# Optimization experiments

Measured on AMD Instinct MI355X. Metric: run time of the kernel, lower is better.

## Reference

```python
import jax, jax.numpy as jnp
import numpy as np

H = 128  # hidden size
IN = 12  # input size
OUT = 4  # output classes


def _lstm_scan(gates_x, Whh, B, dtype, collect_ys):
    """gates_x: [T,B,4H] precomputed input-to-hidden gates (with biases).
    PyTorch gate order: i, f, g, o."""
    h0 = jnp.zeros((B, H), dtype)
    c0 = jnp.zeros((B, H), dtype)

    def step(carry, gx):
        h, c = carry
        g = gx + h @ Whh.T  # [B,4H]
        i, f, gg, o = jnp.split(g, 4, axis=-1)
        c = jax.nn.sigmoid(f) * c + jax.nn.sigmoid(i) * jnp.tanh(gg)
        h = jax.nn.sigmoid(o) * jnp.tanh(c)
        return (h, c), (h if collect_ys else None)

    (hT, cT), hs = jax.lax.scan(step, (h0, c0), gates_x)
    return hs, hT


def setup_inputs() -> dict:
    key = jax.random.key(0)
    ks = jax.random.split(key, 12)
    B, T = 256, 2048
    s = 1.0 / np.sqrt(H)  # torch LSTM/Linear init scale
    u = lambda k, shape: jax.random.uniform(k, shape, jnp.float32, -s, s)
    return {
        "x": jax.random.normal(ks[0], (B, T, IN), jnp.float32),
        "W_ih_l0": u(ks[1], (4 * H, IN)),
        "W_hh_l0": u(ks[2], (4 * H, H)),
        "b_ih_l0": u(ks[3], (4 * H,)),
        "b_hh_l0": u(ks[4], (4 * H,)),
        "W_ih_l1": u(ks[5], (4 * H, H)),
        "W_hh_l1": u(ks[6], (4 * H, H)),
        "b_ih_l1": u(ks[7], (4 * H,)),
        "b_hh_l1": u(ks[8], (4 * H,)),
        "W_out": u(ks[9], (OUT, H)),
        "b_out": u(ks[10], (OUT,)),
    }


def reference(x, W_ih_l0, W_hh_l0, b_ih_l0, b_hh_l0,
              W_ih_l1, W_hh_l1, b_ih_l1, b_hh_l1, W_out, b_out):
    B = x.shape[0]
    # layer 0: precompute all input projections at once -> [T,B,4H]
    gx0 = jnp.einsum('bti,gi->tbg', x, W_ih_l0) + b_ih_l0 + b_hh_l0
    hs0, _ = _lstm_scan(gx0, W_hh_l0, B, x.dtype, collect_ys=True)  # [T,B,H]
    # layer 1: only final hidden state is needed (r_out[:, -1] == h_T)
    gx1 = jnp.einsum('tbh,gh->tbg', hs0, W_ih_l1) + b_ih_l1 + b_hh_l1
    _, hT = _lstm_scan(gx1, W_hh_l1, B, x.dtype, collect_ys=False)  # [B,H]
    return hT @ W_out.T + b_out  # [B,4]
```

## Files before the change

kernel.cpp:

```cpp
#include <hip/hip_runtime.h>
#include <cstdint>
#include <cstddef>

#define H      128
#define IN_    12
#define GATES  512
#define B_     256
#define T_     2048
#define TCMAX  512
#define TS     32


__device__ __forceinline__ float sigmoidf_(float x) {
    return 1.f / (1.f + __expf(-x));
}
__device__ __forceinline__ float tanhf_(float x) {
    return 2.f / (1.f + __expf(-2.f * x)) - 1.f;
}

__global__ __launch_bounds__(512, 1) void lstm_l0(
    const float* __restrict__ x, const float* __restrict__ Wih,
    const float* __restrict__ Whh, const float* __restrict__ bih,
    const float* __restrict__ bhh, float* __restrict__ hs0,
    float* __restrict__ state, int tc, int chunk)
{
    const int b = blockIdx.x;
    const int g = threadIdx.x;

    __shared__ alignas(16) float sh_x[TCMAX * IN_];
    __shared__ alignas(16) float sh_h[H];
    __shared__ alignas(16) float sh_act[GATES];

    float wh[H];
    const float4* wr = (const float4*)(Whh + (size_t)g * H);
#pragma unroll
    for (int k = 0; k < H / 4; ++k) {
        float4 v = wr[k];
        wh[4*k] = v.x; wh[4*k+1] = v.y; wh[4*k+2] = v.z; wh[4*k+3] = v.w;
    }
    float wi[IN_];
    const float4* wr2 = (const float4*)(Wih + (size_t)g * IN_);
#pragma unroll
    for (int k = 0; k < IN_ / 4; ++k) {
        float4 v = wr2[k];
        wi[4*k] = v.x; wi[4*k+1] = v.y; wi[4*k+2] = v.z; wi[4*k+3] = v.w;
    }
    const float bias = bih[g] + bhh[g];

    const float* xs = x + ((size_t)b * T_ + (size_t)chunk * tc) * IN_;
    for (int i = g; i < tc * IN_; i += 512) sh_x[i] = xs[i];

    float hreg = 0.f, creg = 0.f;
    if (g < H) {
        if (chunk) { hreg = state[b * 2 * H + g]; creg = state[b * 2 * H + H + g]; }
        sh_h[g] = hreg;
    }
    __syncthreads();

    float* hs_out = hs0 + (size_t)b * tc * H;

    for (int t = 0; t < tc; ++t) {
        float a0 = bias, a1 = 0.f, a2 = 0.f, a3 = 0.f;
        const float4* xh = (const float4*)(sh_x + t * IN_);
        {
            float4 v = xh[0];
            a0 = fmaf(wi[0], v.x, a0); a1 = fmaf(wi[1], v.y, a1);
            a2 = fmaf(wi[2], v.z, a2); a3 = fmaf(wi[3], v.w, a3);
            v = xh[1];
            a0 = fmaf(wi[4], v.x, a0); a1 = fmaf(wi[5], v.y, a1);
            a2 = fmaf(wi[6], v.z, a2); a3 = fmaf(wi[7], v.w, a3);
            v = xh[2];
            a0 = fmaf(wi[8], v.x, a0); a1 = fmaf(wi[9], v.y, a1);
            a2 = fmaf(wi[10], v.z, a2); a3 = fmaf(wi[11], v.w, a3);
        }
        const float4* h4 = (const float4*)sh_h;
#pragma unroll
        for (int k = 0; k < H / 4; ++k) {
            float4 v = h4[k];
            a0 = fmaf(wh[4*k],   v.x, a0); a1 = fmaf(wh[4*k+1], v.y, a1);
            a2 = fmaf(wh[4*k+2], v.z, a2); a3 = fmaf(wh[4*k+3], v.w, a3);
        }
        float pre = (a0 + a1) + (a2 + a3);
        float act = ((g >> 7) == 2) ? tanhf_(pre) : sigmoidf_(pre);
        sh_act[g] = act;
        __syncthreads();
        if (g < H) {
            creg = fmaf(sh_act[H + g], creg, sh_act[g] * sh_act[2 * H + g]);
            hreg = sh_act[3 * H + g] * tanhf_(creg);
            sh_h[g] = hreg;
            hs_out[(size_t)t * H + g] = hreg;
        }
        __syncthreads();
    }
    if (g < H) { state[b * 2 * H + g] = hreg; state[b * 2 * H + H + g] = creg; }
}

__global__ __launch_bounds__(512, 1) void lstm_l1(
    const float* __restrict__ hs0, const float* __restrict__ Wih,
    const float* __restrict__ Whh, const float* __restrict__ bih,
    const float* __restrict__ bhh, float* __restrict__ state,
    int tc, int chunk)
{
    const int b = blockIdx.x;
    const int g = threadIdx.x;

    __shared__ alignas(16) float sh_h0[TS * H];
    __shared__ alignas(16) float sh_gx[TS * GATES];
    __shared__ alignas(16) float sh_h[H];
    __shared__ alignas(16) float sh_act[GATES];

    float wh[H];
    const float4* wr = (const float4*)(Whh + (size_t)g * H);
#pragma unroll
    for (int k = 0; k < H / 4; ++k) {
        float4 v = wr[k];
        wh[4*k] = v.x; wh[4*k+1] = v.y; wh[4*k+2] = v.z; wh[4*k+3] = v.w;
    }
    const float bias = bih[g] + bhh[g];

    float hreg = 0.f, creg = 0.f;
    if (g < H) {
        if (chunk) { hreg = state[b * 2 * H + g]; creg = state[b * 2 * H + H + g]; }
        sh_h[g] = hreg;
    }
    __syncthreads();

    const float* hsrc = hs0 + (size_t)b * tc * H;
    const float4* wihrow = (const float4*)(Wih + (size_t)g * H);

    const int nsub = tc / TS;
    for (int s = 0; s < nsub; ++s) {
        const float4* src4 = (const float4*)(hsrc + (size_t)s * TS * H);
        float4* dst4 = (float4*)sh_h0;
        for (int i = g; i < TS * H / 4; i += 512) dst4[i] = src4[i];
        __syncthreads();

        float acc[TS];
#pragma unroll
        for (int t = 0; t < TS; ++t) acc[t] = bias;
        for (int k = 0; k < H / 4; ++k) {
            float4 w = wihrow[k];
            const float* hb = sh_h0 + 4 * k;
#pragma unroll
            for (int t = 0; t < TS; ++t) {
                float4 hv = *(const float4*)(hb + t * H);
                acc[t] = fmaf(w.x, hv.x,
                         fmaf(w.y, hv.y,
                         fmaf(w.z, hv.z,
                         fmaf(w.w, hv.w, acc[t]))));
            }
        }
#pragma unroll
        for (int t = 0; t < TS; ++t) sh_gx[t * GATES + g] = acc[t];
        __syncthreads();

        for (int t = 0; t < TS; ++t) {
            float a0 = sh_gx[t * GATES + g], a1 = 0.f, a2 = 0.f, a3 = 0.f;
            const float4* h4 = (const float4*)sh_h;
#pragma unroll
            for (int k = 0; k < H / 4; ++k) {
                float4 v = h4[k];
                a0 = fmaf(wh[4*k],   v.x, a0); a1 = fmaf(wh[4*k+1], v.y, a1);
                a2 = fmaf(wh[4*k+2], v.z, a2); a3 = fmaf(wh[4*k+3], v.w, a3);
            }
            float pre = (a0 + a1) + (a2 + a3);
            float act = ((g >> 7) == 2) ? tanhf_(pre) : sigmoidf_(pre);
            sh_act[g] = act;
            __syncthreads();
            if (g < H) {
                creg = fmaf(sh_act[H + g], creg, sh_act[g] * sh_act[2 * H + g]);
                hreg = sh_act[3 * H + g] * tanhf_(creg);
                sh_h[g] = hreg;
            }
            __syncthreads();
        }
    }
    if (g < H) { state[b * 2 * H + g] = hreg; state[b * 2 * H + H + g] = creg; }
}

__global__ void out_proj(const float* __restrict__ state1,
                         const float* __restrict__ Wout,
                         const float* __restrict__ bout,
                         float* __restrict__ out)
{
    const int b = blockIdx.x, j = threadIdx.x;
    __shared__ float sh[H];
    if (j < H) sh[j] = state1[b * 2 * H + j];
    __syncthreads();
    if (j < 4) {
        float a = bout[j];
        for (int k = 0; k < H; ++k) a = fmaf(Wout[j * H + k], sh[k], a);
        out[b * 4 + j] = a;
    }
}

extern "C" void kernel_launch(void* const* d_in, const int* in_sizes, int n_in,
                              void* d_out, int out_size, void* d_ws, size_t ws_size,
                              hipStream_t stream)
{
    const float* x    = (const float*)d_in[0];
    const float* Wih0 = (const float*)d_in[1];
    const float* Whh0 = (const float*)d_in[2];
    const float* bih0 = (const float*)d_in[3];
    const float* bhh0 = (const float*)d_in[4];
    const float* Wih1 = (const float*)d_in[5];
    const float* Whh1 = (const float*)d_in[6];
    const float* bih1 = (const float*)d_in[7];
    const float* bhh1 = (const float*)d_in[8];
    const float* Wout = (const float*)d_in[9];
    const float* bout = (const float*)d_in[10];

    int tc = 32;
    for (int cand = TCMAX; cand >= 32; cand >>= 1) {
        size_t need = (size_t)B_ * cand * H * 4 + (size_t)B_ * 2 * H * 4 * 2;
        if (need <= ws_size) { tc = cand; break; }
    }

    float* ws  = (float*)d_ws;
    float* hs0 = ws;
    float* st0 = ws + (size_t)B_ * tc * H;
    float* st1 = st0 + (size_t)B_ * 2 * H;

    const int nchunks = T_ / tc;
    for (int c = 0; c < nchunks; ++c) {
        lstm_l0<<<B_, 512, 0, stream>>>(x, Wih0, Whh0, bih0, bhh0, hs0, st0, tc, c);
        lstm_l1<<<B_, 512, 0, stream>>>(hs0, Wih1, Whh1, bih1, bhh1, st1, tc, c);
    }
    out_proj<<<B_, 128, 0, stream>>>(st1, Wout, bout, (float*)d_out);
}
```

Baseline: 5.747 ms.

## Broadcast hidden state via readlane instead of LDS reads in LSTM kernels

In the recurrent step, each wave now reads the hidden state once as a float2 per lane and broadcasts elements with `__builtin_amdgcn_readlane`. This replaces 32 LDS float4 broadcast reads per step, which sit on the serial critical path. The layer-1 input projection drops its `sh_h0` shared staging and the barrier that followed it. Instead, each lane loads one hidden element per timestep and the values are broadcast with readlane into 32 named accumulators. It trades LDS latency for many more scalar readlane instructions and higher register pressure, with waves_per_eu pinned to 2.

```diff
diff --git a/kernel.cpp b/kernel.cpp
--- a/kernel.cpp
+++ b/kernel.cpp
@@ -10,6 +10,17 @@
 #define TCMAX  512
 #define TS     32
 
+#define REP32(M) M(0) M(1) M(2) M(3) M(4) M(5) M(6) M(7) M(8) M(9) M(10) M(11) \
+  M(12) M(13) M(14) M(15) M(16) M(17) M(18) M(19) M(20) M(21) M(22) M(23) \
+  M(24) M(25) M(26) M(27) M(28) M(29) M(30) M(31)
+
+#define RLF(v, l) __int_as_float(__builtin_amdgcn_readlane(__float_as_int(v), (l)))
+
+#define QUAD(j) { \
+    float s0 = RLF(hl.x, 2*j), s1 = RLF(hl.y, 2*j); \
+    float s2 = RLF(hl.x, 2*j+1), s3 = RLF(hl.y, 2*j+1); \
+    a0 = fmaf(w##j.x, s0, a0); a1 = fmaf(w##j.y, s1, a1); \
+    a2 = fmaf(w##j.z, s2, a2); a3 = fmaf(w##j.w, s3, a3); }
 
 __device__ __forceinline__ float sigmoidf_(float x) {
     return 1.f / (1.f + __expf(-x));
@@ -18,33 +29,26 @@
     return 2.f / (1.f + __expf(-2.f * x)) - 1.f;
 }
 
-__global__ __launch_bounds__(512, 1) void lstm_l0(
-    const float* __restrict__ x, const float* __restrict__ Wih,
-    const float* __restrict__ Whh, const float* __restrict__ bih,
-    const float* __restrict__ bhh, float* __restrict__ hs0,
-    float* __restrict__ state, int tc, int chunk)
+__global__ __launch_bounds__(512)
+__attribute__((amdgpu_waves_per_eu(2, 2)))
+void lstm_l0(const float* __restrict__ x, const float* __restrict__ Wih,
+             const float* __restrict__ Whh, const float* __restrict__ bih,
+             const float* __restrict__ bhh, float* __restrict__ hs0,
+             float* __restrict__ state, int tc, int chunk)
 {
     const int b = blockIdx.x;
     const int g = threadIdx.x;
+    const int lane = g & 63;
 
     __shared__ alignas(16) float sh_x[TCMAX * IN_];
-    __shared__ alignas(16) float sh_h[H];
-    __shared__ alignas(16) float sh_act[GATES];
-
-    float wh[H];
-    const float4* wr = (const float4*)(Whh + (size_t)g * H);
-#pragma unroll
-    for (int k = 0; k < H / 4; ++k) {
-        float4 v = wr[k];
-        wh[4*k] = v.x; wh[4*k+1] = v.y; wh[4*k+2] = v.z; wh[4*k+3] = v.w;
-    }
-    float wi[IN_];
+    __shared__ alignas(8)  float sh_h[H];
+    __shared__ float sh_act[GATES];
+
+#define LW(j) float4 w##j = ((const float4*)(Whh + (size_t)g * H))[j];
+    REP32(LW)
+#undef LW
     const float4* wr2 = (const float4*)(Wih + (size_t)g * IN_);
-#pragma unroll
-    for (int k = 0; k < IN_ / 4; ++k) {
-        float4 v = wr2[k];
-        wi[4*k] = v.x; wi[4*k+1] = v.y; wi[4*k+2] = v.z; wi[4*k+3] = v.w;
-    }
+    float4 wiA = wr2[0], wiB = wr2[1], wiC = wr2[2];
     const float bias = bih[g] + bhh[g];
 
     const float* xs = x + ((size_t)b * T_ + (size_t)chunk * tc) * IN_;
@@ -60,26 +64,17 @@
     float* hs_out = hs0 + (size_t)b * tc * H;
 
     for (int t = 0; t < tc; ++t) {
+        float2 hl = ((const float2*)sh_h)[lane];
         float a0 = bias, a1 = 0.f, a2 = 0.f, a3 = 0.f;
         const float4* xh = (const float4*)(sh_x + t * IN_);
-        {
-            float4 v = xh[0];
-            a0 = fmaf(wi[0], v.x, a0); a1 = fmaf(wi[1], v.y, a1);
-            a2 = fmaf(wi[2], v.z, a2); a3 = fmaf(wi[3], v.w, a3);
-            v = xh[1];
-            a0 = fmaf(wi[4], v.x, a0); a1 = fmaf(wi[5], v.y, a1);
-            a2 = fmaf(wi[6], v.z, a2); a3 = fmaf(wi[7], v.w, a3);
-            v = xh[2];
-            a0 = fmaf(wi[8], v.x, a0); a1 = fmaf(wi[9], v.y, a1);
-            a2 = fmaf(wi[10], v.z, a2); a3 = fmaf(wi[11], v.w, a3);
-        }
-        const float4* h4 = (const float4*)sh_h;
-#pragma unroll
-        for (int k = 0; k < H / 4; ++k) {
-            float4 v = h4[k];
-            a0 = fmaf(wh[4*k],   v.x, a0); a1 = fmaf(wh[4*k+1], v.y, a1);
-            a2 = fmaf(wh[4*k+2], v.z, a2); a3 = fmaf(wh[4*k+3], v.w, a3);
-        }
+        float4 xv0 = xh[0], xv1 = xh[1], xv2 = xh[2];
+        a0 = fmaf(wiA.x, xv0.x, a0); a1 = fmaf(wiA.y, xv0.y, a1);
+        a2 = fmaf(wiA.z, xv0.z, a2); a3 = fmaf(wiA.w, xv0.w, a3);
+        a0 = fmaf(wiB.x, xv1.x, a0); a1 = fmaf(wiB.y, xv1.y, a1);
+        a2 = fmaf(wiB.z, xv1.z, a2); a3 = fmaf(wiB.w, xv1.w, a3);
+        a0 = fmaf(wiC.x, xv2.x, a0); a1 = fmaf(wiC.y, xv2.y, a1);
+        a2 = fmaf(wiC.z, xv2.z, a2); a3 = fmaf(wiC.w, xv2.w, a3);
+        REP32(QUAD)
         float pre = (a0 + a1) + (a2 + a3);
         float act = ((g >> 7) == 2) ? tanhf_(pre) : sigmoidf_(pre);
         sh_act[g] = act;
@@ -95,27 +90,24 @@
     if (g < H) { state[b * 2 * H + g] = hreg; state[b * 2 * H + H + g] = creg; }
 }
 
-__global__ __launch_bounds__(512, 1) void lstm_l1(
-    const float* __restrict__ hs0, const float* __restrict__ Wih,
-    const float* __restrict__ Whh, const float* __restrict__ bih,
-    const float* __restrict__ bhh, float* __restrict__ state,
-    int tc, int chunk)
+__global__ __launch_bounds__(512)
+__attribute__((amdgpu_waves_per_eu(2, 2)))
+void lstm_l1(const float* __restrict__ hs0, const float* __restrict__ Wih,
+             const float* __restrict__ Whh, const float* __restrict__ bih,
+             const float* __restrict__ bhh, float* __restrict__ state,
+             int tc, int chunk)
 {
     const int b = blockIdx.x;
     const int g = threadIdx.x;
-
-    __shared__ alignas(16) float sh_h0[TS * H];
-    __shared__ alignas(16) float sh_gx[TS * GATES];
-    __shared__ alignas(16) float sh_h[H];
-    __shared__ alignas(16) float sh_act[GATES];
-
-    float wh[H];
-    const float4* wr = (const float4*)(Whh + (size_t)g * H);
-#pragma unroll
-    for (int k = 0; k < H / 4; ++k) {
-        float4 v = wr[k];
-        wh[4*k] = v.x; wh[4*k+1] = v.y; wh[4*k+2] = v.z; wh[4*k+3] = v.w;
-    }
+    const int lane = g & 63;
+
+    __shared__ float sh_gx[TS * GATES];
+    __shared__ alignas(8) float sh_h[H];
+    __shared__ float sh_act[GATES];
+
+#define LW(j) float4 w##j = ((const float4*)(Whh + (size_t)g * H))[j];
+    REP32(LW)
+#undef LW
     const float bias = bih[g] + bhh[g];
 
     float hreg = 0.f, creg = 0.f;
@@ -128,41 +120,49 @@
     const float* hsrc = hs0 + (size_t)b * tc * H;
     const float4* wihrow = (const float4*)(Wih + (size_t)g * H);
 
-    const int nsub = tc / TS;
-    for (int s = 0; s < nsub; ++s) {
-        const float4* src4 = (const float4*)(hsrc + (size_t)s * TS * H);
-        float4* dst4 = (float4*)sh_h0;
-        for (int i = g; i < TS * H / 4; i += 512) dst4[i] = src4[i];
-        __syncthreads();
-
-        float acc[TS];
-#pragma unroll
-        for (int t = 0; t < TS; ++t) acc[t] = bias;
-        for (int k = 0; k < H / 4; ++k) {
-            float4 w = wihrow[k];
-            const float* hb = sh_h0 + 4 * k;
-#pragma unroll
-            for (int t = 0; t < TS; ++t) {
-                float4 hv = *(const float4*)(hb + t * H);
-                acc[t] = fmaf(w.x, hv.x,
-                         fmaf(w.y, hv.y,
-                         fmaf(w.z, hv.z,
-                         fmaf(w.w, hv.w, acc[t]))));
-            }
-        }
-#pragma unroll
-        for (int t = 0; t < TS; ++t) sh_gx[t * GATES + g] = acc[t];
-        __syncthreads();
+    for (int s = 0; s < tc / TS; ++s) {
+        const float* hsA = hsrc + (size_t)s * TS * H;
+
+#define DECL(t) float dA##t;
+        REP32(DECL)
+#undef DECL
+#define ACC(t) float ac##t = bias;
+        REP32(ACC)
+#undef ACC
+#define LTA(t) dA##t = hsA[t * H + lane];
+        REP32(LTA)
+#undef LTA
+        for (int k4 = 0; k4 < 16; ++k4) {
+            float4 wq = wihrow[k4];
+            int kl = 4 * k4;
+#define PA(t) { ac##t = fmaf(wq.x, RLF(dA##t, kl),     ac##t); \
+                ac##t = fmaf(wq.y, RLF(dA##t, kl + 1), ac##t); \
+                ac##t = fmaf(wq.z, RLF(dA##t, kl + 2), ac##t); \
+                ac##t = fmaf(wq.w, RLF(dA##t, kl + 3), ac##t); }
+            REP32(PA)
+#undef PA
+        }
+#define LTB(t) dA##t = hsA[t * H + 64 + lane];
+        REP32(LTB)
+#undef LTB
+        for (int k4 = 16; k4 < 32; ++k4) {
+            float4 wq = wihrow[k4];
+            int kl = 4 * k4 - 64;
+#define PB(t) { ac##t = fmaf(wq.x, RLF(dA##t, kl),     ac##t); \
+                ac##t = fmaf(wq.y, RLF(dA##t, kl + 1), ac##t); \
+                ac##t = fmaf(wq.z, RLF(dA##t, kl + 2), ac##t); \
+                ac##t = fmaf(wq.w, RLF(dA##t, kl + 3), ac##t); }
+            REP32(PB)
+#undef PB
+        }
+#define ST(t) sh_gx[t * GATES + g] = ac##t;
+        REP32(ST)
+#undef ST
 
         for (int t = 0; t < TS; ++t) {
+            float2 hl = ((const float2*)sh_h)[lane];
             float a0 = sh_gx[t * GATES + g], a1 = 0.f, a2 = 0.f, a3 = 0.f;
-            const float4* h4 = (const float4*)sh_h;
-#pragma unroll
-            for (int k = 0; k < H / 4; ++k) {
-                float4 v = h4[k];
-                a0 = fmaf(wh[4*k],   v.x, a0); a1 = fmaf(wh[4*k+1], v.y, a1);
-                a2 = fmaf(wh[4*k+2], v.z, a2); a3 = fmaf(wh[4*k+3], v.w, a3);
-            }
+            REP32(QUAD)
             float pre = (a0 + a1) + (a2 + a3);
             float act = ((g >> 7) == 2) ? tanhf_(pre) : sigmoidf_(pre);
             sh_act[g] = act;
```

Result: slower. 7.427 ms (+29.2%).

## Split recurrent matvec over 1024 threads and move layer-1 input GEMM to separate kernel

Applied to the files above, without the earlier changes.

The recurrent scan kernel now uses 1024 threads per batch row. Each thread computes a 16-wide K-slice partial for four gate rows, and the partials are reduced through padded shared memory by 128 threads, which also apply the fused gate activations. The layer-1 input projection moves out of the serial scan into a separate gx1_gemm kernel gridded over batch and time tiles, writing a gx workspace that the scan prefetches one step ahead. This cuts per-thread serial FMA depth on the recurrence critical path. In exchange it adds a shared-memory reduction each step, extra global traffic for gx1, and a larger workspace that may shrink the chunk size.

```diff
diff --git a/kernel.cpp b/kernel.cpp
--- a/kernel.cpp
+++ b/kernel.cpp
@@ -8,8 +8,12 @@
 #define B_     256
 #define T_     2048
 #define TCMAX  512
-#define TS     32
-
+#define TI     32
+#define PS     520
+
+#define REP32(M) M(0) M(1) M(2) M(3) M(4) M(5) M(6) M(7) M(8) M(9) M(10) M(11) \
+  M(12) M(13) M(14) M(15) M(16) M(17) M(18) M(19) M(20) M(21) M(22) M(23) \
+  M(24) M(25) M(26) M(27) M(28) M(29) M(30) M(31)
 
 __device__ __forceinline__ float sigmoidf_(float x) {
     return 1.f / (1.f + __expf(-x));
@@ -17,165 +21,167 @@
 __device__ __forceinline__ float tanhf_(float x) {
     return 2.f / (1.f + __expf(-2.f * x)) - 1.f;
 }
-
-__global__ __launch_bounds__(512, 1) void lstm_l0(
-    const float* __restrict__ x, const float* __restrict__ Wih,
-    const float* __restrict__ Whh, const float* __restrict__ bih,
-    const float* __restrict__ bhh, float* __restrict__ hs0,
-    float* __restrict__ state, int tc, int chunk)
-{
-    const int b = blockIdx.x;
-    const int g = threadIdx.x;
-
-    __shared__ alignas(16) float sh_x[TCMAX * IN_];
-    __shared__ alignas(16) float sh_h[H];
-    __shared__ alignas(16) float sh_act[GATES];
-
-    float wh[H];
-    const float4* wr = (const float4*)(Whh + (size_t)g * H);
-#pragma unroll
-    for (int k = 0; k < H / 4; ++k) {
-        float4 v = wr[k];
-        wh[4*k] = v.x; wh[4*k+1] = v.y; wh[4*k+2] = v.z; wh[4*k+3] = v.w;
-    }
-    float wi[IN_];
-    const float4* wr2 = (const float4*)(Wih + (size_t)g * IN_);
-#pragma unroll
-    for (int k = 0; k < IN_ / 4; ++k) {
-        float4 v = wr2[k];
-        wi[4*k] = v.x; wi[4*k+1] = v.y; wi[4*k+2] = v.z; wi[4*k+3] = v.w;
-    }
-    const float bias = bih[g] + bhh[g];
-
-    const float* xs = x + ((size_t)b * T_ + (size_t)chunk * tc) * IN_;
-    for (int i = g; i < tc * IN_; i += 512) sh_x[i] = xs[i];
-
+__device__ __forceinline__ float dot4f(float4 w, float4 h, float a) {
+    return fmaf(w.x, h.x, fmaf(w.y, h.y, fmaf(w.z, h.z, fmaf(w.w, h.w, a))));
+}
+
+template<bool IS_L0>
+__global__ __launch_bounds__(1024) void lstm_scan(
+    const float* __restrict__ x_or_gx,
+    const float* __restrict__ Wih,
+    const float* __restrict__ Whh,
+    const float* __restrict__ bih, const float* __restrict__ bhh,
+    float* __restrict__ hs0,
+    float* __restrict__ state,
+    int tc, int chunk)
+{
+    const int b   = blockIdx.x;
+    const int tid = threadIdx.x;
+    const int ks  = tid >> 7;
+    const int q   = tid & 127;
+
+    extern __shared__ float smem[];
+    float* sh_part = smem;
+    float* sh_h    = smem + 8 * PS;
+    float* sh_x    = sh_h + H;
+
+#define LOADW(i) \
+    const float4* wr##i = (const float4*)(Whh + (size_t)(4*q+i)*H + 16*ks); \
+    float4 w##i##0 = wr##i[0], w##i##1 = wr##i[1], w##i##2 = wr##i[2], w##i##3 = wr##i[3];
+    LOADW(0) LOADW(1) LOADW(2) LOADW(3)
+#undef LOADW
+
+    float4 wx0 = {0,0,0,0}, wx1 = {0,0,0,0}, wx2 = {0,0,0,0}, wx3 = {0,0,0,0};
+    if constexpr (IS_L0) {
+        if (ks >= 1 && ks <= 3) {
+            wx0 = *(const float4*)(Wih + (size_t)(4*q+0)*IN_ + 4*(ks-1));
+            wx1 = *(const float4*)(Wih + (size_t)(4*q+1)*IN_ + 4*(ks-1));
+            wx2 = *(const float4*)(Wih + (size_t)(4*q+2)*IN_ + 4*(ks-1));
+            wx3 = *(const float4*)(Wih + (size_t)(4*q+3)*IN_ + 4*(ks-1));
+        }
+        const float* xs = x_or_gx + ((size_t)b * T_ + (size_t)chunk * tc) * IN_;
+        for (int i = tid; i < tc * IN_; i += 1024) sh_x[i] = xs[i];
+    }
+
+    float bias0 = 0, bias1 = 0, bias2 = 0, bias3 = 0;
+    float cur0 = 0, cur1 = 0, cur2 = 0, cur3 = 0;
     float hreg = 0.f, creg = 0.f;
-    if (g < H) {
-        if (chunk) { hreg = state[b * 2 * H + g]; creg = state[b * 2 * H + H + g]; }
-        sh_h[g] = hreg;
+    const float* gxb = nullptr;
+    if constexpr (!IS_L0) gxb = x_or_gx + (size_t)b * tc * GATES;
+
+    if (tid < H) {
+        if constexpr (IS_L0) {
+            bias0 = bih[tid]         + bhh[tid];
+            bias1 = bih[tid + 128]   + bhh[tid + 128];
+            bias2 = bih[tid + 256]   + bhh[tid + 256];
+            bias3 = bih[tid + 384]   + bhh[tid + 384];
+        } else {
+            cur0 = gxb[tid]; cur1 = gxb[tid + 128];
+            cur2 = gxb[tid + 256]; cur3 = gxb[tid + 384];
+        }
+        if (chunk) { hreg = state[b*2*H + tid]; creg = state[b*2*H + H + tid]; }
+        sh_h[tid] = hreg;
     }
     __syncthreads();
 
-    float* hs_out = hs0 + (size_t)b * tc * H;
+    float* hs_out = nullptr;
+    if constexpr (IS_L0) hs_out = hs0 + (size_t)b * tc * H;
+
+    const float4* sh4 = (const float4*)sh_h;
+    const int i0 = tid & 3, q0 = tid >> 2;
 
     for (int t = 0; t < tc; ++t) {
-        float a0 = bias, a1 = 0.f, a2 = 0.f, a3 = 0.f;
-        const float4* xh = (const float4*)(sh_x + t * IN_);
-        {
-            float4 v = xh[0];
-            a0 = fmaf(wi[0], v.x, a0); a1 = fmaf(wi[1], v.y, a1);
-            a2 = fmaf(wi[2], v.z, a2); a3 = fmaf(wi[3], v.w, a3);
-            v = xh[1];
-            a0 = fmaf(wi[4], v.x, a0); a1 = fmaf(wi[5], v.y, a1);
-            a2 = fmaf(wi[6], v.z, a2); a3 = fmaf(wi[7], v.w, a3);
-            v = xh[2];
-            a0 = fmaf(wi[8], v.x, a0); a1 = fmaf(wi[9], v.y, a1);
-            a2 = fmaf(wi[10], v.z, a2); a3 = fmaf(wi[11], v.w, a3);
-        }
-        const float4* h4 = (const float4*)sh_h;
-#pragma unroll
-        for (int k = 0; k < H / 4; ++k) {
-            float4 v = h4[k];
-            a0 = fmaf(wh[4*k],   v.x, a0); a1 = fmaf(wh[4*k+1], v.y, a1);
-            a2 = fmaf(wh[4*k+2], v.z, a2); a3 = fmaf(wh[4*k+3], v.w, a3);
-        }
-        float pre = (a0 + a1) + (a2 + a3);
-        float act = ((g >> 7) == 2) ? tanhf_(pre) : sigmoidf_(pre);
-        sh_act[g] = act;
+        float n0 = 0, n1 = 0, n2 = 0, n3 = 0;
+        if constexpr (!IS_L0) {
+            if (tid < H) {
+                int tn = (t + 1 < tc) ? t + 1 : t;
+                const float* gp = gxb + (size_t)tn * GATES;
+                n0 = gp[tid]; n1 = gp[tid + 128];
+                n2 = gp[tid + 256]; n3 = gp[tid + 384];
+            }
+        }
+        float4 hA = sh4[4*ks], hB = sh4[4*ks+1], hC = sh4[4*ks+2], hD = sh4[4*ks+3];
+        float a0 = dot4f(w03,hD, dot4f(w02,hC, dot4f(w01,hB, dot4f(w00,hA, 0.f))));
+        float a1 = dot4f(w13,hD, dot4f(w12,hC, dot4f(w11,hB, dot4f(w10,hA, 0.f))));
+        float a2 = dot4f(w23,hD, dot4f(w22,hC, dot4f(w21,hB, dot4f(w20,hA, 0.f))));
+        float a3 = dot4f(w33,hD, dot4f(w32,hC, dot4f(w31,hB, dot4f(w30,hA, 0.f))));
+        if constexpr (IS_L0) {
+            if (ks >= 1 && ks <= 3) {
+                float4 xq = *(const float4*)(sh_x + t * IN_ + 4*(ks-1));
+                a0 = dot4f(wx0, xq, a0); a1 = dot4f(wx1, xq, a1);
+                a2 = dot4f(wx2, xq, a2); a3 = dot4f(wx3, xq, a3);
+            }
+        }
+        sh_part[ks*PS + 0*128 + q] = a0;
+        sh_part[ks*PS + 1*128 + q] = a1;
+        sh_part[ks*PS + 2*128 + q] = a2;
+        sh_part[ks*PS + 3*128 + q] = a3;
         __syncthreads();
-        if (g < H) {
-            creg = fmaf(sh_act[H + g], creg, sh_act[g] * sh_act[2 * H + g]);
-            hreg = sh_act[3 * H + g] * tanhf_(creg);
-            sh_h[g] = hreg;
-            hs_out[(size_t)t * H + g] = hreg;
+
+        if (tid < H) {
+            float p0, p1, p2, p3;
+            {
+                const float* pb = sh_part + i0*128 + q0;
+#define RSUM(m, dst) { \
+                float s = pb[32*m]; \
+                s += pb[32*m + 1*PS]; s += pb[32*m + 2*PS]; s += pb[32*m + 3*PS]; \
+                s += pb[32*m + 4*PS]; s += pb[32*m + 5*PS]; s += pb[32*m + 6*PS]; \
+                s += pb[32*m + 7*PS]; dst = s; }
+                RSUM(0, p0) RSUM(1, p1) RSUM(2, p2) RSUM(3, p3)
+#undef RSUM
+            }
+            float gi, gf, gg, go;
+            if constexpr (IS_L0) {
+                gi = p0 + bias0; gf = p1 + bias1; gg = p2 + bias2; go = p3 + bias3;
+            } else {
+                gi = p0 + cur0; gf = p1 + cur1; gg = p2 + cur2; go = p3 + cur3;
+                cur0 = n0; cur1 = n1; cur2 = n2; cur3 = n3;
+            }
+            creg = fmaf(sigmoidf_(gf), creg, sigmoidf_(gi) * tanhf_(gg));
+            hreg = sigmoidf_(go) * tanhf_(creg);
+            sh_h[tid] = hreg;
+            if constexpr (IS_L0) hs_out[(size_t)t * H + tid] = hreg;
         }
         __syncthreads();
     }
-    if (g < H) { state[b * 2 * H + g] = hreg; state[b * 2 * H + H + g] = creg; }
-}
-
-__global__ __launch_bounds__(512, 1) void lstm_l1(
+    if (tid < H) { state[b*2*H + tid] = hreg; state[b*2*H + H + tid] = creg; }
+}
+
+__global__ __launch_bounds__(512) void gx1_gemm(
     const float* __restrict__ hs0, const float* __restrict__ Wih,
-    const float* __restrict__ Whh, const float* __restrict__ bih,
-    const float* __restrict__ bhh, float* __restrict__ state,
-    int tc, int chunk)
-{
-    const int b = blockIdx.x;
-    const int g = threadIdx.x;
-
-    __shared__ alignas(16) float sh_h0[TS * H];
-    __shared__ alignas(16) float sh_gx[TS * GATES];
-    __shared__ alignas(16) float sh_h[H];
-    __shared__ alignas(16) float sh_act[GATES];
-
-    float wh[H];
-    const float4* wr = (const float4*)(Whh + (size_t)g * H);
-#pragma unroll
-    for (int k = 0; k < H / 4; ++k) {
-        float4 v = wr[k];
-        wh[4*k] = v.x; wh[4*k+1] = v.y; wh[4*k+2] = v.z; wh[4*k+3] = v.w;
-    }
-    const float bias = bih[g] + bhh[g];
-
-    float hreg = 0.f, creg = 0.f;
-    if (g < H) {
-        if (chunk) { hreg = state[b * 2 * H + g]; creg = state[b * 2 * H + H + g]; }
-        sh_h[g] = hreg;
-    }
+    const float* __restrict__ bih, const float* __restrict__ bhh,
+    float* __restrict__ gx, int tc)
+{
+    const int b  = blockIdx.x;
+    const int t0 = blockIdx.y * TI;
+    const int g  = threadIdx.x;
+
+    __shared__ alignas(16) float sh_h0[TI * H];
+
+    const float4* src4 = (const float4*)(hs0 + ((size_t)b * tc + t0) * H);
+    float4* dst4 = (float4*)sh_h0;
+    for (int i = g; i < TI * H / 4; i += 512) dst4[i] = src4[i];
+
+    const float biasg = bih[g] + bhh[g];
+#define AI(t) float acc##t = biasg;
+    REP32(AI)
+#undef AI
     __syncthreads();
 
-    const float* hsrc = hs0 + (size_t)b * tc * H;
-    const float4* wihrow = (const float4*)(Wih + (size_t)g * H);
-
-    const int nsub = tc / TS;
-    for (int s = 0; s < nsub; ++s) {
-        const float4* src4 = (const float4*)(hsrc + (size_t)s * TS * H);
-        float4* dst4 = (float4*)sh_h0;
-        for (int i = g; i < TS * H / 4; i += 512) dst4[i] = src4[i];
-        __syncthreads();
-
-        float acc[TS];
-#pragma unroll
-        for (int t = 0; t < TS; ++t) acc[t] = bias;
-        for (int k = 0; k < H / 4; ++k) {
-            float4 w = wihrow[k];
-            const float* hb = sh_h0 + 4 * k;
-#pragma unroll
-            for (int t = 0; t < TS; ++t) {
-                float4 hv = *(const float4*)(hb + t * H);
-                acc[t] = fmaf(w.x, hv.x,
-                         fmaf(w.y, hv.y,
-                         fmaf(w.z, hv.z,
-                         fmaf(w.w, hv.w, acc[t]))));
-            }
-        }
-#pragma unroll
-        for (int t = 0; t < TS; ++t) sh_gx[t * GATES + g] = acc[t];
-        __syncthreads();
-
-        for (int t = 0; t < TS; ++t) {
-            float a0 = sh_gx[t * GATES + g], a1 = 0.f, a2 = 0.f, a3 = 0.f;
-            const float4* h4 = (const float4*)sh_h;
-#pragma unroll
-            for (int k = 0; k < H / 4; ++k) {
-                float4 v = h4[k];
-                a0 = fmaf(wh[4*k],   v.x, a0); a1 = fmaf(wh[4*k+1], v.y, a1);
-                a2 = fmaf(wh[4*k+2], v.z, a2); a3 = fmaf(wh[4*k+3], v.w, a3);
-            }
-            float pre = (a0 + a1) + (a2 + a3);
-            float act = ((g >> 7) == 2) ? tanhf_(pre) : sigmoidf_(pre);
-            sh_act[g] = act;
-            __syncthreads();
-            if (g < H) {
-                creg = fmaf(sh_act[H + g], creg, sh_act[g] * sh_act[2 * H + g]);
-                hreg = sh_act[3 * H + g] * tanhf_(creg);
-                sh_h[g] = hreg;
-            }
-            __syncthreads();
-        }
-    }
-    if (g < H) { state[b * 2 * H + g] = hreg; state[b * 2 * H + H + g] = creg; }
+    const float4* wrow = (const float4*)(Wih + (size_t)g * H);
+    const float4* sh4h = (const float4*)sh_h0;
+    for (int k4 = 0; k4 < H / 4; ++k4) {
+        float4 wq = wrow[k4];
+#define PA(t) { float4 hv = sh4h[t*32 + k4]; \
+        acc##t = fmaf(wq.x, hv.x, fmaf(wq.y, hv.y, fmaf(wq.z, hv.z, fmaf(wq.w, hv.w, acc##t)))); }
+        REP32(PA)
+#undef PA
+    }
+
+    float* gxo = gx + (size_t)b * tc * GATES;
+#define SG(t) gxo[(size_t)(t0 + t) * GATES + g] = acc##t;
+    REP32(SG)
+#undef SG
 }
 
 __global__ void out_proj(const float* __restrict__ state1,
@@ -185,12 +191,12 @@
 {
     const int b = blockIdx.x, j = threadIdx.x;
     __shared__ float sh[H];
-    if (j < H) sh[j] = state1[b * 2 * H + j];
+    if (j < H) sh[j] = state1[b*2*H + j];
     __syncthreads();
     if (j < 4) {
         float a = bout[j];
-        for (int k = 0; k < H; ++k) a = fmaf(Wout[j * H + k], sh[k], a);
-        out[b * 4 + j] = a;
+        for (int k = 0; k < H; ++k) a = fmaf(Wout[j*H + k], sh[k], a);
+        out[b*4 + j] = a;
     }
 }
 
@@ -212,19 +218,29 @@
 
     int tc = 32;
     for (int cand = TCMAX; cand >= 32; cand >>= 1) {
-        size_t need = (size_t)B_ * cand * H * 4 + (size_t)B_ * 2 * H * 4 * 2;
+        size_t need = (size_t)2 * B_ * 2 * H * 4
+                    + (size_t)B_ * cand * H * 4
+                    + (size_t)B_ * cand * GATES * 4;
         if (need <= ws_size) { tc = cand; break; }
     }
 
     float* ws  = (float*)d_ws;
-    float* hs0 = ws;
-    float* st0 = ws + (size_t)B_ * tc * H;
+    float* st0 = ws;
     float* st1 = st0 + (size_t)B_ * 2 * H;
+    float* hs0 = st1 + (size_t)B_ * 2 * H;
+    float* gx1 = hs0 + (size_t)B_ * tc * H;
+
+    const size_t shm_l0 = (size_t)(8 * PS + H + tc * IN_) * 4;
+    const size_t shm_l1 = (size_t)(8 * PS + H) * 4;
 
     const int nchunks = T_ / tc;
     for (int c = 0; c < nchunks; ++c) {
-        lstm_l0<<<B_, 512, 0, stream>>>(x, Wih0, Whh0, bih0, bhh0, hs0, st0, tc, c);
-        lstm_l1<<<B_, 512, 0, stream>>>(hs0, Wih1, Whh1, bih1, bhh1, st1, tc, c);
+        lstm_scan<true><<<B_, 1024, shm_l0, stream>>>(
+            x, Wih0, Whh0, bih0, bhh0, hs0, st0, tc, c);
+        gx1_gemm<<<dim3(B_, tc / TI), 512, 0, stream>>>(
+            hs0, Wih1, bih1, bhh1, gx1, tc);
+        lstm_scan<false><<<B_, 1024, shm_l1, stream>>>(
+            gx1, nullptr, Whh1, nullptr, nullptr, nullptr, st1, tc, c);
     }
     out_proj<<<B_, 128, 0, stream>>>(st1, Wout, bout, (float*)d_out);
 }
```

New measurement: 5.247 ms. 1.1x faster.
